# Kernel optimization log

Hardware: AMD Instinct MI355X
Metric: run time of the kernel (lower is better)

## Reference

```python
import jax, jax.numpy as jnp
import numpy as np

B, H, S, D = 1, 16, 2048, 128
SINK = 4            # SINK_LENGTH in source
QMAX = 7.0          # 4-bit symmetric: 2**(4-1)-1
K_OUT = 8           # outlier tokens kept per (b,h,d) channel slice (outlier_dim=-2)
V_OUT = 4           # outlier channels kept per (b,h,s) token slice (outlier_dim=-1)


def setup_inputs() -> dict:
    key = jax.random.key(0)
    kq, kk, kv = jax.random.split(key, 3)
    return {
        "q_tensor": jax.random.normal(kq, (B, H, S, D), jnp.float32),
        "k_tensor": jax.random.normal(kk, (B, H, S, D), jnp.float32),
        "v_tensor": jax.random.normal(kv, (B, H, S, D), jnp.float32),
    }


def _causal_attention(q, k, v):
    # standard SDPA, prefill chunk (cache empty), no RoPE (rotary_emb_module is None)
    scores = jnp.einsum("bhqd,bhkd->bhqk", q, k) * (D ** -0.5)
    causal = jnp.tril(jnp.ones((S, S), bool))
    scores = jnp.where(causal, scores, -1e30)
    probs = jax.nn.softmax(scores, axis=-1)
    return jnp.einsum("bhqk,bhkd->bhqd", probs, v)


def _isolate_k(x, n):
    # outlier_dim=-2: per (b,h,d) channel slice, pull top-n |.| tokens out as sparse
    xt = jnp.transpose(x, (0, 1, 3, 2))                     # [B,H,D,S]
    _, idx = jax.lax.top_k(jnp.abs(xt), n)                  # [B,H,D,n] token indices
    vals = jnp.take_along_axis(xt, idx, axis=-1)            # [B,H,D,n]
    bb = jnp.arange(B)[:, None, None, None]
    hh = jnp.arange(H)[None, :, None, None]
    dd = jnp.arange(D)[None, None, :, None]
    dense = jnp.transpose(xt.at[bb, hh, dd, idx].set(0.0), (0, 1, 3, 2))
    flat_idx = ((bb * H + hh) * S + idx) * D + dd           # flat index into [B,H,S,D]
    return dense, vals.reshape(-1), flat_idx.reshape(-1)


def _isolate_v(x, n):
    # outlier_dim=-1: per (b,h,s) token slice, pull top-n |.| channels out as sparse
    _, idx = jax.lax.top_k(jnp.abs(x), n)                   # [B,H,S,n] channel indices
    vals = jnp.take_along_axis(x, idx, axis=-1)
    bb = jnp.arange(B)[:, None, None, None]
    hh = jnp.arange(H)[None, :, None, None]
    ss = jnp.arange(S)[None, None, :, None]
    dense = x.at[bb, hh, ss, idx].set(0.0)
    flat_idx = ((bb * H + hh) * S + ss) * D + idx
    return dense, vals.reshape(-1), flat_idx.reshape(-1)


def _quantize_dense(x, absmax):
    scale = jnp.maximum(absmax, 1e-8) / QMAX
    q = jnp.clip(jnp.round(x / scale), -QMAX, QMAX)
    return q, scale


def reference(q_tensor, k_tensor, v_tensor):
    attn_output = _causal_attention(q_tensor, k_tensor, v_tensor)

    # chunk 0 prefill: zero sink tokens before outlier isolation
    k_iso = k_tensor.at[:, :, :SINK, :].set(0.0)
    v_iso = v_tensor.at[:, :, :SINK, :].set(0.0)

    k_dense, k_sp_val, k_sp_idx = _isolate_k(k_iso, K_OUT)
    v_dense, v_sp_val, v_sp_idx = _isolate_v(v_iso, V_OUT)

    # append full-precision sink tokens as sparse entries (flat indices)
    flat_ids = jnp.arange(B * H * S * D, dtype=jnp.int32).reshape(B, H, S, D)
    sink_idx = flat_ids[:, :, :SINK, :].reshape(-1)
    v_sp_val = jnp.concatenate([v_sp_val, v_tensor[:, :, :SINK, :].reshape(-1)])
    v_sp_idx = jnp.concatenate([v_sp_idx.astype(jnp.int32), sink_idx])
    k_sp_val = jnp.concatenate([k_sp_val, k_tensor[:, :, :SINK, :].reshape(-1)])
    k_sp_idx = jnp.concatenate([k_sp_idx.astype(jnp.int32), sink_idx])

    # key stats: per-channel absmax over tokens; value stats: per-token absmax over channels
    k_absmax = jnp.max(jnp.abs(k_dense), axis=2, keepdims=True)   # [B,H,1,D]
    v_absmax = jnp.max(jnp.abs(v_dense), axis=3, keepdims=True)   # [B,H,S,1]

    k_quant, k_scale = _quantize_dense(k_dense, k_absmax)
    v_quant, v_scale = _quantize_dense(v_dense, v_absmax)

    return (attn_output,
            k_quant, k_scale, k_sp_val, k_sp_idx,
            v_quant, v_scale, v_sp_val, v_sp_idx)
```

## Files before the change

kernel.cpp:

```cpp
#include <hip/hip_runtime.h>

#define HH 16
#define SS 2048
#define DD 128

#define O0 0u
#define O1 4194304u
#define O2 8388608u
#define O3 8390656u
#define O4 8415232u
#define O5 8439808u
#define O6 12634112u
#define O7 12666880u
#define O8 12806144u

using bf16x8 = __attribute__((ext_vector_type(8))) short;
using f32x4  = __attribute__((ext_vector_type(4))) float;

static __device__ __forceinline__ unsigned short f2bf(float f) {
  union { float f; unsigned u; } x; x.f = f;
  unsigned r = x.u + 0x7fffu + ((x.u >> 16) & 1u);
  return (unsigned short)(r >> 16);
}

typedef __attribute__((address_space(1))) const unsigned int gu32_t;
typedef __attribute__((address_space(3))) unsigned int lu32_t;
static __device__ __forceinline__ void gl_lds16(const void* g, void* l) {
  __builtin_amdgcn_global_load_lds((gu32_t*)g, (lu32_t*)l, 16, 0, 0);
}

#define INS9(a_, v_, i_)                                              \
  if ((a_) > aab[8]) {                                                \
    aab[8] = (a_); av[8] = (v_); ai[8] = (i_);                        \
    _Pragma("unroll")                                                 \
    for (int jj = 8; jj > 0; --jj) {                                  \
      if (aab[jj] > aab[jj - 1]) {                                    \
        float ta = aab[jj]; aab[jj] = aab[jj - 1]; aab[jj - 1] = ta;  \
        float tv = av[jj];  av[jj]  = av[jj - 1];  av[jj - 1]  = tv;  \
        int   ti = ai[jj];  ai[jj]  = ai[jj - 1];  ai[jj - 1]  = ti;  \
      }                                                               \
    }                                                                 \
  }

#define INS5(a_, v_, i_)                                              \
  if ((a_) > ab5[4]) {                                                \
    ab5[4] = (a_); v5[4] = (v_); i5[4] = (i_);                        \
    _Pragma("unroll")                                                 \
    for (int jj = 4; jj > 0; --jj) {                                  \
      if (ab5[jj] > ab5[jj - 1]) {                                    \
        float ta = ab5[jj]; ab5[jj] = ab5[jj - 1]; ab5[jj - 1] = ta;  \
        float tv = v5[jj];  v5[jj]  = v5[jj - 1];  v5[jj - 1]  = tv;  \
        int   ti = i5[jj];  i5[jj]  = i5[jj - 1];  i5[jj - 1]  = ti;  \
      }                                                               \
    }                                                                 \
  }

__global__ __launch_bounds__(256) void prep_kv(const float* __restrict__ K,
                                               const float* __restrict__ V,
                                               uint4* __restrict__ WK,
                                               uint4* __restrict__ WV,
                                               float* __restrict__ wval,
                                               int* __restrict__ widx,
                                               float* __restrict__ out) {
  if (blockIdx.y == 0) {
    if (blockIdx.x >= 256) return;
    const int h  = blockIdx.x >> 4;
    const int sb = blockIdx.x & 15;
    const float* Kh = K + (size_t)h * (SS * DD);
    const int tid = threadIdx.x;

    for (int slot = tid; slot < 2048; slot += 256) {
      const int tl = slot >> 10, sl = slot & 1023;
      const int chunk = sl >> 6, l = sl & 63;
      const int ct = chunk >> 2, t = chunk & 3;
      const int row = (sb * 2 + tl) * 64 + ct * 16 + (l & 15);
      const float* src = Kh + (size_t)row * DD + t * 32 + (l >> 4) * 8;
      const float4 a = *(const float4*)src;
      const float4 b = *(const float4*)(src + 4);
      uint4 r;
      r.x = (unsigned)f2bf(a.x) | ((unsigned)f2bf(a.y) << 16);
      r.y = (unsigned)f2bf(a.z) | ((unsigned)f2bf(a.w) << 16);
      r.z = (unsigned)f2bf(b.x) | ((unsigned)f2bf(b.y) << 16);
      r.w = (unsigned)f2bf(b.z) | ((unsigned)f2bf(b.w) << 16);
      WK[(size_t)(h * 32 + sb * 2 + tl) * 1024 + sl] = r;
    }

    const int d   = tid & 127;
    const int sub = tid >> 7;
    const int s0  = sb * 128 + sub * 64;
    float aab[9], av[9]; int ai[9];
    #pragma unroll
    for (int j = 0; j < 9; ++j) { aab[j] = -1.f; av[j] = 0.f; ai[j] = 0; }
    for (int ib = 0; ib < 64; ib += 8) {
      float vv[8];
      #pragma unroll
      for (int u = 0; u < 8; ++u)
        vv[u] = Kh[((size_t)(s0 + ib + u) << 7) + d];
      #pragma unroll
      for (int u = 0; u < 8; ++u) {
        const int s = s0 + ib + u;
        const float v = (s < 4) ? 0.f : vv[u];
        const float a = fabsf(v);
        INS9(a, v, s)
      }
    }
    __shared__ float lv[128][9];
    __shared__ int   li[128][9];
    if (sub == 1) {
      #pragma unroll
      for (int j = 0; j < 9; ++j) { lv[d][j] = av[j]; li[d][j] = ai[j]; }
    }
    __syncthreads();
    if (sub == 0) {
      #pragma unroll
      for (int j = 0; j < 9; ++j) {
        const float v = lv[d][j];
        const int  s2 = li[d][j];
        const float a = fabsf(v);
        INS9(a, v, s2)
      }
      const int base = (sb * 2048 + h * 128 + d) * 9;
      #pragma unroll
      for (int j = 0; j < 9; ++j) { wval[base + j] = av[j]; widx[base + j] = ai[j]; }
    }
  } else {
    __shared__ float T[64][133];
    __shared__ float pv[64][4][5];
    __shared__ int   pi[64][4][5];
    __shared__ float ssc[64];
    __shared__ int   sid4[64][4];
    const int ht = blockIdx.x;
    const int h = ht >> 5;
    const int s_base = (ht & 31) * 64;
    const float* Vh = V + (size_t)h * (SS * DD) + (size_t)s_base * DD;

    for (int i = threadIdx.x; i < 2048; i += 256) {
      const int flat = i << 2;
      const int row = flat >> 7, col = flat & 127;
      const float4 a = *(const float4*)(Vh + (size_t)row * DD + col);
      T[row][col]     = a.x;
      T[row][col + 1] = a.y;
      T[row][col + 2] = a.z;
      T[row][col + 3] = a.w;
    }
    __syncthreads();

    uint4* dst = WV + (size_t)ht * 1024;
    for (int slot = threadIdx.x; slot < 1024; slot += 256) {
      const int chunk = slot >> 6, l = slot & 63;
      const int c = chunk >> 1, tk = chunk & 1;
      const int n  = c * 16 + (l & 15);
      const int k0 = tk * 32 + (l >> 4) * 8;
      unsigned short u[8];
      #pragma unroll
      for (int j = 0; j < 8; ++j) u[j] = f2bf(T[k0 + j][n]);
      uint4 r;
      r.x = (unsigned)u[0] | ((unsigned)u[1] << 16);
      r.y = (unsigned)u[2] | ((unsigned)u[3] << 16);
      r.z = (unsigned)u[4] | ((unsigned)u[5] << 16);
      r.w = (unsigned)u[6] | ((unsigned)u[7] << 16);
      dst[slot] = r;
    }

    {
      const int tok  = threadIdx.x >> 2;
      const int part = threadIdx.x & 3;
      const int sg   = s_base + tok;
      float ab5[5], v5[5]; int i5[5];
      #pragma unroll
      for (int j = 0; j < 5; ++j) { ab5[j] = -1.f; v5[j] = 0.f; i5[j] = 0; }
      for (int c = 0; c < 32; ++c) {
        const int ch = part * 32 + c;
        const float w = (sg < 4) ? 0.f : T[tok][ch];
        const float a = fabsf(w);
        INS5(a, w, ch)
      }
      #pragma unroll
      for (int j = 0; j < 5; ++j) { pv[tok][part][j] = v5[j]; pi[tok][part][j] = i5[j]; }
    }
    __syncthreads();

    if (threadIdx.x < 64) {
      const int tok = threadIdx.x;
      const int sg  = s_base + tok;
      float ab5[5], v5[5]; int i5[5];
      #pragma unroll
      for (int j = 0; j < 5; ++j) { ab5[j] = -1.f; v5[j] = 0.f; i5[j] = 0; }
      for (int part = 0; part < 4; ++part)
        #pragma unroll
        for (int j = 0; j < 5; ++j) {
          const float w = pv[tok][part][j];
          const int  ch = pi[tok][part][j];
          const float a = fabsf(w);
          INS5(a, w, ch)
        }
      const float scale = fmaxf(ab5[4], 1e-8f) / 7.0f;
      const int gw = h * SS + sg;
      out[O6 + gw] = scale;
      ssc[tok] = scale;
      #pragma unroll
      for (int j = 0; j < 4; ++j) {
        out[O7 + gw * 4 + j] = v5[j];
        out[O8 + gw * 4 + j] = (float)(gw * DD + i5[j]);
        sid4[tok][j] = i5[j];
      }
    }
    __syncthreads();

    for (int e = threadIdx.x; e < 8192; e += 256) {
      const int tok = e >> 7, ch = e & 127;
      const int sg  = s_base + tok;
      const float w = (sg < 4) ? 0.f : T[tok][ch];
      const bool z = (ch == sid4[tok][0]) | (ch == sid4[tok][1]) |
                     (ch == sid4[tok][2]) | (ch == sid4[tok][3]);
      const float q = z ? 0.f : fminf(7.f, fmaxf(-7.f, rintf(w / ssc[tok])));
      out[O5 + (size_t)(h * SS + sg) * DD + ch] = q;
    }
  }
}

__global__ __launch_bounds__(256) void attn_ws(const float* __restrict__ Q,
                                               const uint4* __restrict__ WK,
                                               const uint4* __restrict__ WV,
                                               float* __restrict__ O) {
  const int bid = blockIdx.x;
  const int x  = bid & 7;
  const int kk = bid >> 3;
  const int p  = kk >> 5;
  const int r  = kk & 31;
  const int h  = x * 2 + (r & 1);
  const int jj = r >> 1;
  const int qb = p ? (31 - jj) : jj;
  const int q0 = qb << 6;
  const int tid = threadIdx.x;
  const int w   = tid >> 6;
  const int l   = tid & 63;
  const int l15 = l & 15;
  const int lg  = l >> 4;

  __shared__ uint4 Kt[2][1024];
  __shared__ uint4 Vt[2][1024];
  __shared__ unsigned short Pl[4][16][72];

  bf16x8 qf[4];
  {
    const float* qp = Q + (size_t)h * (SS * DD) + (size_t)(q0 + w * 16 + l15) * DD + lg * 8;
    #pragma unroll
    for (int t = 0; t < 4; ++t) {
      const float4 a = *(const float4*)(qp + t * 32);
      const float4 b = *(const float4*)(qp + t * 32 + 4);
      bf16x8 f;
      f[0] = (short)f2bf(a.x); f[1] = (short)f2bf(a.y);
      f[2] = (short)f2bf(a.z); f[3] = (short)f2bf(a.w);
      f[4] = (short)f2bf(b.x); f[5] = (short)f2bf(b.y);
      f[6] = (short)f2bf(b.z); f[7] = (short)f2bf(b.w);
      qf[t] = f;
    }
  }

  f32x4 acc[8];
  #pragma unroll
  for (int c = 0; c < 8; ++c) acc[c] = (f32x4){0.f, 0.f, 0.f, 0.f};
  float mrow = -1e30f, lrow = 0.f;

  const float sc2 = 0.08838834764831845f * 1.4426950408889634f;

  {
    const size_t tbase = (size_t)(h * 32) * 1024;
    #pragma unroll
    for (int i = 0; i < 4; ++i) {
      const int ch = (w << 2) + i;
      gl_lds16(WK + tbase + ch * 64 + l, &Kt[0][ch * 64]);
      gl_lds16(WV + tbase + ch * 64 + l, &Vt[0][ch * 64]);
    }
  }
  __syncthreads();

  for (int kt = 0; kt <= qb; ++kt) {
    const int cur = kt & 1;

    if (kt < qb) {
      const size_t tbase = (size_t)(h * 32 + kt + 1) * 1024;
      #pragma unroll
      for (int i = 0; i < 4; ++i) {
        const int ch = (w << 2) + i;
        gl_lds16(WK + tbase + ch * 64 + l, &Kt[cur ^ 1][ch * 64]);
        gl_lds16(WV + tbase + ch * 64 + l, &Vt[cur ^ 1][ch * 64]);
      }
    }

    const bool diag = (kt == qb);
    const int ctmax = diag ? (w + 1) : 4;

    float p[4][4];
    float mt = -1e30f;
    __builtin_amdgcn_s_setprio(1);
    #pragma unroll
    for (int ct = 0; ct < 4; ++ct) {
      if (ct < ctmax) {
        f32x4 a = (f32x4){0.f, 0.f, 0.f, 0.f};
        #pragma unroll
        for (int t = 0; t < 4; ++t) {
          bf16x8 kb = ((const bf16x8*)Kt[cur])[(ct * 4 + t) * 64 + l];
          a = __builtin_amdgcn_mfma_f32_16x16x32_bf16(kb, qf[t], a, 0, 0, 0);
        }
        #pragma unroll
        for (int r2 = 0; r2 < 4; ++r2) {
          float s = a[r2] * sc2;
          if (diag) {
            const int koff = ct * 16 + lg * 4 + r2;
            s = (koff > w * 16 + l15) ? -1e30f : s;
          }
          p[ct][r2] = s;
          mt = fmaxf(mt, s);
        }
      }
    }
    __builtin_amdgcn_s_setprio(0);

    mt = fmaxf(mt, __shfl_xor(mt, 16));
    mt = fmaxf(mt, __shfl_xor(mt, 32));
    const float mn = fmaxf(mrow, mt);

    float rs = 0.f;
    #pragma unroll
    for (int ct = 0; ct < 4; ++ct) {
      if (ct < ctmax) {
        #pragma unroll
        for (int r2 = 0; r2 < 4; ++r2) {
          const float e = exp2f(p[ct][r2] - mn);
          p[ct][r2] = e;
          rs += e;
        }
      } else {
        #pragma unroll
        for (int r2 = 0; r2 < 4; ++r2) p[ct][r2] = 0.f;
      }
    }
    rs += __shfl_xor(rs, 16);
    rs += __shfl_xor(rs, 32);

    if (__any(mt > mrow)) {
      const float al = exp2f(mrow - mn);
      float alr[4];
      #pragma unroll
      for (int r2 = 0; r2 < 4; ++r2) alr[r2] = __shfl(al, lg * 4 + r2);
      #pragma unroll
      for (int c = 0; c < 8; ++c)
        #pragma unroll
        for (int r2 = 0; r2 < 4; ++r2) acc[c][r2] *= alr[r2];
      lrow = lrow * al + rs;
      mrow = mn;
    } else {
      lrow += rs;
    }

    #pragma unroll
    for (int ct = 0; ct < 4; ++ct) {
      uint2 pk;
      pk.x = (unsigned)f2bf(p[ct][0]) | ((unsigned)f2bf(p[ct][1]) << 16);
      pk.y = (unsigned)f2bf(p[ct][2]) | ((unsigned)f2bf(p[ct][3]) << 16);
      *(uint2*)&Pl[w][l15][ct * 16 + lg * 4] = pk;
    }

    __builtin_amdgcn_s_setprio(1);
    #pragma unroll
    for (int tk = 0; tk < 2; ++tk) {
      bf16x8 pa = *(const bf16x8*)&Pl[w][l15][tk * 32 + lg * 8];
      #pragma unroll
      for (int c = 0; c < 8; ++c) {
        bf16x8 vb = ((const bf16x8*)Vt[cur])[(c * 2 + tk) * 64 + l];
        acc[c] = __builtin_amdgcn_mfma_f32_16x16x32_bf16(pa, vb, acc[c], 0, 0, 0);
      }
    }
    __builtin_amdgcn_s_setprio(0);

    __syncthreads();
  }

  const float inv = 1.0f / lrow;
  float invr[4];
  #pragma unroll
  for (int r2 = 0; r2 < 4; ++r2) invr[r2] = __shfl(inv, lg * 4 + r2);
  #pragma unroll
  for (int r2 = 0; r2 < 4; ++r2) {
    const int row = q0 + w * 16 + lg * 4 + r2;
    float* op = O + O0 + (size_t)(h * SS + row) * DD;
    #pragma unroll
    for (int c = 0; c < 8; ++c)
      op[c * 16 + l15] = acc[c][r2] * invr[r2];
  }
}

__global__ __launch_bounds__(256) void attn_fb(const float* __restrict__ Q,
                                               const float* __restrict__ K,
                                               const float* __restrict__ V,
                                               float* __restrict__ O) {
  const int h   = blockIdx.x >> 5;
  const int q0  = (blockIdx.x & 31) << 6;
  const int tid = threadIdx.x;
  const int w   = tid >> 6;
  const int l   = tid & 63;
  const int l15 = l & 15;
  const int lg  = l >> 4;

  __shared__ unsigned short Kl[64][136];
  __shared__ unsigned short Vt[128][72];
  __shared__ unsigned short Pl[4][16][72];

  const size_t hbase = (size_t)h * (SS * DD);
  const float* Qh = Q + hbase;
  const float* Kh = K + hbase;
  const float* Vh = V + hbase;

  bf16x8 qf[4];
  {
    const float* qp = Qh + (size_t)(q0 + w * 16 + l15) * DD + lg * 8;
    #pragma unroll
    for (int t = 0; t < 4; ++t) {
      bf16x8 f;
      #pragma unroll
      for (int j = 0; j < 8; ++j) f[j] = (short)f2bf(qp[t * 32 + j]);
      qf[t] = f;
    }
  }

  f32x4 acc[8];
  #pragma unroll
  for (int c = 0; c < 8; ++c) acc[c] = (f32x4){0.f, 0.f, 0.f, 0.f};
  float mrow[4], lrow[4];
  #pragma unroll
  for (int r = 0; r < 4; ++r) { mrow[r] = -1e30f; lrow[r] = 0.f; }

  const float sc2 = 0.08838834764831845f * 1.4426950408889634f;

  const int ntile = (q0 >> 6) + 1;
  for (int kt = 0; kt < ntile; ++kt) {
    const int kv0 = kt << 6;
    __syncthreads();
    for (int idx = tid; idx < 64 * 128; idx += 256) {
      const int kv = idx >> 7, d = idx & 127;
      const size_t g = (size_t)(kv0 + kv) * DD + d;
      Kl[kv][d] = f2bf(Kh[g]);
      Vt[d][kv] = f2bf(Vh[g]);
    }
    __syncthreads();

    f32x4 sacc[4];
    #pragma unroll
    for (int ct = 0; ct < 4; ++ct) {
      f32x4 a = (f32x4){0.f, 0.f, 0.f, 0.f};
      #pragma unroll
      for (int t = 0; t < 4; ++t) {
        bf16x8 kb = *(const bf16x8*)&Kl[ct * 16 + l15][t * 32 + lg * 8];
        a = __builtin_amdgcn_mfma_f32_16x16x32_bf16(qf[t], kb, a, 0, 0, 0);
      }
      sacc[ct] = a;
    }

    float sv[4][4];
    #pragma unroll
    for (int ct = 0; ct < 4; ++ct) {
      const int col = kv0 + ct * 16 + l15;
      #pragma unroll
      for (int r = 0; r < 4; ++r) {
        const int row = q0 + w * 16 + lg * 4 + r;
        sv[ct][r] = (col > row) ? -1e30f : sacc[ct][r] * sc2;
      }
    }

    #pragma unroll
    for (int r = 0; r < 4; ++r) {
      float mt = fmaxf(fmaxf(sv[0][r], sv[1][r]), fmaxf(sv[2][r], sv[3][r]));
      #pragma unroll
      for (int m = 1; m < 16; m <<= 1) mt = fmaxf(mt, __shfl_xor(mt, m));
      const float mn = fmaxf(mrow[r], mt);
      const float al = exp2f(mrow[r] - mn);
      mrow[r] = mn;
      float rs = 0.f;
      #pragma unroll
      for (int ct = 0; ct < 4; ++ct) {
        const float p = exp2f(sv[ct][r] - mn);
        sv[ct][r] = p;
        rs += p;
      }
      #pragma unroll
      for (int m = 1; m < 16; m <<= 1) rs += __shfl_xor(rs, m);
      lrow[r] = lrow[r] * al + rs;
      #pragma unroll
      for (int c = 0; c < 8; ++c) acc[c][r] *= al;
    }

    #pragma unroll
    for (int ct = 0; ct < 4; ++ct)
      #pragma unroll
      for (int r = 0; r < 4; ++r)
        Pl[w][lg * 4 + r][ct * 16 + l15] = f2bf(sv[ct][r]);

    #pragma unroll
    for (int tk = 0; tk < 2; ++tk) {
      bf16x8 pa = *(const bf16x8*)&Pl[w][l15][tk * 32 + lg * 8];
      #pragma unroll
      for (int c = 0; c < 8; ++c) {
        bf16x8 vb = *(const bf16x8*)&Vt[c * 16 + l15][tk * 32 + lg * 8];
        acc[c] = __builtin_amdgcn_mfma_f32_16x16x32_bf16(pa, vb, acc[c], 0, 0, 0);
      }
    }
  }

  #pragma unroll
  for (int r = 0; r < 4; ++r) {
    const float inv = 1.0f / lrow[r];
    const int row = q0 + w * 16 + lg * 4 + r;
    float* op = O + O0 + (size_t)(h * SS + row) * DD;
    #pragma unroll
    for (int c = 0; c < 8; ++c)
      op[c * 16 + l15] = acc[c][r] * inv;
  }
}

__global__ __launch_bounds__(256) void v_kernel(const float* __restrict__ V,
                                                float* __restrict__ out) {
  const int gw = (blockIdx.x << 2) + (threadIdx.x >> 6);
  const int l  = threadIdx.x & 63;
  const int s  = gw & (SS - 1);
  const float2 v2 = ((const float2*)(V + (size_t)gw * DD))[l];
  const bool sink = (s < 4);
  const float w0 = sink ? 0.f : v2.x;
  const float w1 = sink ? 0.f : v2.y;
  float a0 = fabsf(w0), a1 = fabsf(w1);
  const int d0 = 2 * l, d1 = 2 * l + 1;

  float oval[4]; int oidx[4]; float scale = 0.f;
  #pragma unroll
  for (int rnd = 0; rnd < 5; ++rnd) {
    float ba; int bd; float bv;
    if (a1 > a0) { ba = a1; bd = d1; bv = w1; }
    else         { ba = a0; bd = d0; bv = w0; }
    #pragma unroll
    for (int m = 1; m < 64; m <<= 1) {
      const float oa = __shfl_xor(ba, m);
      const int   od = __shfl_xor(bd, m);
      const float ov = __shfl_xor(bv, m);
      if (oa > ba || (oa == ba && od < bd)) { ba = oa; bd = od; bv = ov; }
    }
    if (rnd < 4) {
      oval[rnd] = bv; oidx[rnd] = bd;
      if (bd == d0) a0 = -1.f;
      if (bd == d1) a1 = -1.f;
    } else {
      scale = fmaxf(ba, 1e-8f) / 7.0f;
    }
  }

  const bool z0 = (oidx[0] == d0) | (oidx[1] == d0) | (oidx[2] == d0) | (oidx[3] == d0);
  const bool z1 = (oidx[0] == d1) | (oidx[1] == d1) | (oidx[2] == d1) | (oidx[3] == d1);
  const float q0 = z0 ? 0.f : fminf(7.f, fmaxf(-7.f, rintf(w0 / scale)));
  const float q1 = z1 ? 0.f : fminf(7.f, fmaxf(-7.f, rintf(w1 / scale)));
  float2 pack; pack.x = q0; pack.y = q1;
  *(float2*)(out + O5 + (size_t)gw * DD + d0) = pack;

  if (l == 0) {
    out[O6 + gw] = scale;
    #pragma unroll
    for (int j = 0; j < 4; ++j) {
      out[O7 + gw * 4 + j] = oval[j];
      out[O8 + gw * 4 + j] = (float)(gw * DD + oidx[j]);
    }
  }
}

__global__ __launch_bounds__(64) void k_merge(const float* __restrict__ wval,
                                              const int* __restrict__ widx,
                                              const float* __restrict__ K,
                                              const float* __restrict__ V,
                                              float* __restrict__ out) {
  const int ch = blockIdx.x * 64 + threadIdx.x;
  const int h = ch >> 7, d = ch & 127;

  float aab[9], av[9]; int ai[9];
  #pragma unroll
  for (int j = 0; j < 9; ++j) { aab[j] = -1.f; av[j] = 0.f; ai[j] = 0; }

  float va[9], vb[9]; int ia[9], ib[9];
  {
    const int b0 = ch * 9;
    #pragma unroll
    for (int j = 0; j < 9; ++j) { va[j] = wval[b0 + j]; ia[j] = widx[b0 + j]; }
  }

  for (int sb = 0; sb < 16; ++sb) {
    if (sb < 15) {
      const int nb = ((sb + 1) * 2048 + ch) * 9;
      #pragma unroll
      for (int j = 0; j < 9; ++j) { vb[j] = wval[nb + j]; ib[j] = widx[nb + j]; }
    }
    #pragma unroll
    for (int j = 0; j < 9; ++j) {
      const float v = va[j];
      const int  si = ia[j];
      const float a = fabsf(v);
      INS9(a, v, si)
    }
    #pragma unroll
    for (int j = 0; j < 9; ++j) { va[j] = vb[j]; ia[j] = ib[j]; }
  }

  const float scale = fmaxf(aab[8], 1e-8f) / 7.0f;
  out[O2 + ch] = scale;
  #pragma unroll
  for (int j = 0; j < 8; ++j) {
    out[O3 + ch * 8u + j] = av[j];
    out[O4 + ch * 8u + j] = (float)((h * SS + ai[j]) * DD + d);
  }

  #pragma unroll
  for (int u = 0; u < 4; ++u) {
    const int i  = ch * 4 + u;
    const int hh = i >> 9;
    const int r  = i & 511;
    const int flat = hh * (SS * DD) + r;
    const float fidx = (float)flat;
    out[O3 + 16384u + i]  = K[flat];
    out[O4 + 16384u + i]  = fidx;
    out[O7 + 131072u + i] = V[flat];
    out[O8 + 131072u + i] = fidx;
  }
}

__global__ __launch_bounds__(256) void k_top(const float* __restrict__ K,
                                             float* __restrict__ out) {
  const int h  = blockIdx.x;
  const int t  = threadIdx.x;
  const int st = t >> 7;
  const float* Kh = K + (size_t)h * (SS * DD);

  __shared__ float lv[256][9];
  __shared__ int   li[256][9];

  float aab[9], av[9]; int ai[9];
  #pragma unroll
  for (int j = 0; j < 9; ++j) { aab[j] = -1.f; av[j] = 0.f; ai[j] = 0; }

  const int d = t & 127;
  const int s0 = st << 10;
  for (int i = 0; i < 1024; ++i) {
    const int s = s0 + i;
    float v = Kh[((size_t)s << 7) + d];
    if (s < 4) v = 0.f;
    const float a = fabsf(v);
    INS9(a, v, s)
  }

  #pragma unroll
  for (int j = 0; j < 9; ++j) { lv[t][j] = av[j]; li[t][j] = ai[j]; }
  __syncthreads();

  if (t < 128) {
    #pragma unroll
    for (int j = 0; j < 9; ++j) {
      const float v = lv[t + 128][j];
      const int  s2 = li[t + 128][j];
      const float a = fabsf(v);
      INS9(a, v, s2)
    }
    const float scale = fmaxf(aab[8], 1e-8f) / 7.0f;
    const unsigned ch = (unsigned)(h * 128 + t);
    out[O2 + ch] = scale;
    #pragma unroll
    for (int j = 0; j < 8; ++j) {
      out[O3 + ch * 8u + j] = av[j];
      out[O4 + ch * 8u + j] = (float)((h * SS + ai[j]) * DD + t);
    }
  }
}

__global__ __launch_bounds__(256) void sink_kernel(const float* __restrict__ K,
                                                   const float* __restrict__ V,
                                                   float* __restrict__ out) {
  const int i = blockIdx.x * 256 + threadIdx.x;
  const int h = i >> 9;
  const int r = i & 511;
  const int flat = h * (SS * DD) + r;
  const float fidx = (float)flat;
  out[O3 + 16384u + i]  = K[flat];
  out[O4 + 16384u + i]  = fidx;
  out[O7 + 131072u + i] = V[flat];
  out[O8 + 131072u + i] = fidx;
}

__global__ __launch_bounds__(256) void k_quant(const float* __restrict__ K,
                                               const float* __restrict__ outr,
                                               float* __restrict__ out) {
  __shared__ float ssc[128];
  __shared__ int   sid[128][8];
  const int e0 = blockIdx.x * 1024;
  const int h  = e0 >> 18;
  if (threadIdx.x < 128) {
    const unsigned ch = (unsigned)(h * 128 + threadIdx.x);
    ssc[threadIdx.x] = outr[O2 + ch];
    #pragma unroll
    for (int j = 0; j < 8; ++j)
      sid[threadIdx.x][j] = ((int)outr[O4 + ch * 8u + j] >> 7) & (SS - 1);
  }
  __syncthreads();

  const int e  = e0 + threadIdx.x * 4;
  const int dd = e & 127;
  const int s  = (e >> 7) & (SS - 1);
  const float4 kv = *(const float4*)(K + e);
  const float vv[4] = {kv.x, kv.y, kv.z, kv.w};
  float4 res;
  float rr[4];
  #pragma unroll
  for (int jj = 0; jj < 4; ++jj) {
    const int d = dd + jj;
    bool zero = (s < 4);
    #pragma unroll
    for (int j = 0; j < 8; ++j) zero |= (sid[d][j] == s);
    rr[jj] = zero ? 0.f : fminf(7.f, fmaxf(-7.f, rintf(vv[jj] / ssc[d])));
  }
  res.x = rr[0]; res.y = rr[1]; res.z = rr[2]; res.w = rr[3];
  *(float4*)(out + O1 + e) = res;
}

extern "C" void kernel_launch(void* const* d_in, const int* in_sizes, int n_in,
                              void* d_out, int out_size, void* d_ws, size_t ws_size,
                              hipStream_t stream) {
  const float* q = (const float*)d_in[0];
  const float* k = (const float*)d_in[1];
  const float* v = (const float*)d_in[2];
  float* out = (float*)d_out;

  const size_t nBF   = 524288;
  const size_t nPart = (size_t)2048 * 16 * 9;
  const size_t needFull = nBF * 2 * sizeof(uint4) + nPart * 8;

  uint4* wsk = (uint4*)d_ws;
  uint4* wsv = wsk + nBF;
  float* wval = (float*)(wsv + nBF);
  int*   widx = (int*)(wval + nPart);

  if (ws_size >= needFull) {
    prep_kv<<<dim3(512, 2), dim3(256), 0, stream>>>(k, v, wsk, wsv, wval, widx, out);
    attn_ws<<<dim3(512), dim3(256), 0, stream>>>(q, wsk, wsv, out);
    k_merge<<<dim3(32), dim3(64), 0, stream>>>(wval, widx, k, v, out);
  } else {
    attn_fb<<<dim3(512), dim3(256), 0, stream>>>(q, k, v, out);
    v_kernel<<<dim3(HH * SS / 4), dim3(256), 0, stream>>>(v, out);
    k_top<<<dim3(HH), dim3(256), 0, stream>>>(k, out);
    sink_kernel<<<dim3(32), dim3(256), 0, stream>>>(k, v, out);
  }
  k_quant<<<dim3(4096), dim3(256), 0, stream>>>(k, out, out);
}
```

Measured before the change: 202.0 us.

## Split fused K/V prep kernel and move V top-k quantization to warp-per-token kernel

The combined prep_kv kernel is split into prep_k (K bf16 packing plus partial top-k) and prep_v (V bf16 transpose-pack only). V outlier extraction and quantization move to the existing warp-per-token v_kernel, which now runs after attention. The aim is to take the serial per-token insertion sorts and the extra block syncs out of the prep stage so attention's inputs are ready sooner. The cost is one more kernel launch and V being read from global memory a second time.

```diff
diff --git a/kernel.cpp b/kernel.cpp
--- a/kernel.cpp
+++ b/kernel.cpp
@@ -42,179 +42,153 @@
     }                                                                 \
   }
 
-#define INS5(a_, v_, i_)                                              \
-  if ((a_) > ab5[4]) {                                                \
-    ab5[4] = (a_); v5[4] = (v_); i5[4] = (i_);                        \
-    _Pragma("unroll")                                                 \
-    for (int jj = 4; jj > 0; --jj) {                                  \
-      if (ab5[jj] > ab5[jj - 1]) {                                    \
-        float ta = ab5[jj]; ab5[jj] = ab5[jj - 1]; ab5[jj - 1] = ta;  \
-        float tv = v5[jj];  v5[jj]  = v5[jj - 1];  v5[jj - 1]  = tv;  \
-        int   ti = i5[jj];  i5[jj]  = i5[jj - 1];  i5[jj - 1]  = ti;  \
-      }                                                               \
-    }                                                                 \
-  }
-
-__global__ __launch_bounds__(256) void prep_kv(const float* __restrict__ K,
-                                               const float* __restrict__ V,
-                                               uint4* __restrict__ WK,
-                                               uint4* __restrict__ WV,
-                                               float* __restrict__ wval,
-                                               int* __restrict__ widx,
-                                               float* __restrict__ out) {
-  if (blockIdx.y == 0) {
-    if (blockIdx.x >= 256) return;
-    const int h  = blockIdx.x >> 4;
-    const int sb = blockIdx.x & 15;
-    const float* Kh = K + (size_t)h * (SS * DD);
-    const int tid = threadIdx.x;
-
-    for (int slot = tid; slot < 2048; slot += 256) {
-      const int tl = slot >> 10, sl = slot & 1023;
-      const int chunk = sl >> 6, l = sl & 63;
-      const int ct = chunk >> 2, t = chunk & 3;
-      const int row = (sb * 2 + tl) * 64 + ct * 16 + (l & 15);
-      const float* src = Kh + (size_t)row * DD + t * 32 + (l >> 4) * 8;
-      const float4 a = *(const float4*)src;
-      const float4 b = *(const float4*)(src + 4);
-      uint4 r;
-      r.x = (unsigned)f2bf(a.x) | ((unsigned)f2bf(a.y) << 16);
-      r.y = (unsigned)f2bf(a.z) | ((unsigned)f2bf(a.w) << 16);
-      r.z = (unsigned)f2bf(b.x) | ((unsigned)f2bf(b.y) << 16);
-      r.w = (unsigned)f2bf(b.z) | ((unsigned)f2bf(b.w) << 16);
-      WK[(size_t)(h * 32 + sb * 2 + tl) * 1024 + sl] = r;
-    }
-
-    const int d   = tid & 127;
-    const int sub = tid >> 7;
-    const int s0  = sb * 128 + sub * 64;
-    float aab[9], av[9]; int ai[9];
-    #pragma unroll
-    for (int j = 0; j < 9; ++j) { aab[j] = -1.f; av[j] = 0.f; ai[j] = 0; }
-    for (int ib = 0; ib < 64; ib += 8) {
-      float vv[8];
-      #pragma unroll
-      for (int u = 0; u < 8; ++u)
-        vv[u] = Kh[((size_t)(s0 + ib + u) << 7) + d];
-      #pragma unroll
-      for (int u = 0; u < 8; ++u) {
-        const int s = s0 + ib + u;
-        const float v = (s < 4) ? 0.f : vv[u];
-        const float a = fabsf(v);
-        INS9(a, v, s)
-      }
-    }
-    __shared__ float lv[128][9];
-    __shared__ int   li[128][9];
-    if (sub == 1) {
-      #pragma unroll
-      for (int j = 0; j < 9; ++j) { lv[d][j] = av[j]; li[d][j] = ai[j]; }
-    }
-    __syncthreads();
-    if (sub == 0) {
-      #pragma unroll
-      for (int j = 0; j < 9; ++j) {
-        const float v = lv[d][j];
-        const int  s2 = li[d][j];
-        const float a = fabsf(v);
-        INS9(a, v, s2)
-      }
-      const int base = (sb * 2048 + h * 128 + d) * 9;
-      #pragma unroll
-      for (int j = 0; j < 9; ++j) { wval[base + j] = av[j]; widx[base + j] = ai[j]; }
-    }
-  } else {
-    __shared__ float T[64][133];
-    __shared__ float pv[64][4][5];
-    __shared__ int   pi[64][4][5];
-    __shared__ float ssc[64];
-    __shared__ int   sid4[64][4];
-    const int ht = blockIdx.x;
-    const int h = ht >> 5;
-    const int s_base = (ht & 31) * 64;
-    const float* Vh = V + (size_t)h * (SS * DD) + (size_t)s_base * DD;
-
-    for (int i = threadIdx.x; i < 2048; i += 256) {
-      const int flat = i << 2;
-      const int row = flat >> 7, col = flat & 127;
-      const float4 a = *(const float4*)(Vh + (size_t)row * DD + col);
-      T[row][col]     = a.x;
-      T[row][col + 1] = a.y;
-      T[row][col + 2] = a.z;
-      T[row][col + 3] = a.w;
-    }
-    __syncthreads();
-
-    uint4* dst = WV + (size_t)ht * 1024;
-    for (int slot = threadIdx.x; slot < 1024; slot += 256) {
-      const int chunk = slot >> 6, l = slot & 63;
-      const int c = chunk >> 1, tk = chunk & 1;
-      const int n  = c * 16 + (l & 15);
-      const int k0 = tk * 32 + (l >> 4) * 8;
-      unsigned short u[8];
-      #pragma unroll
-      for (int j = 0; j < 8; ++j) u[j] = f2bf(T[k0 + j][n]);
-      uint4 r;
-      r.x = (unsigned)u[0] | ((unsigned)u[1] << 16);
-      r.y = (unsigned)u[2] | ((unsigned)u[3] << 16);
-      r.z = (unsigned)u[4] | ((unsigned)u[5] << 16);
-      r.w = (unsigned)u[6] | ((unsigned)u[7] << 16);
-      dst[slot] = r;
-    }
-
-    {
-      const int tok  = threadIdx.x >> 2;
-      const int part = threadIdx.x & 3;
-      const int sg   = s_base + tok;
-      float ab5[5], v5[5]; int i5[5];
-      #pragma unroll
-      for (int j = 0; j < 5; ++j) { ab5[j] = -1.f; v5[j] = 0.f; i5[j] = 0; }
-      for (int c = 0; c < 32; ++c) {
-        const int ch = part * 32 + c;
-        const float w = (sg < 4) ? 0.f : T[tok][ch];
-        const float a = fabsf(w);
-        INS5(a, w, ch)
-      }
-      #pragma unroll
-      for (int j = 0; j < 5; ++j) { pv[tok][part][j] = v5[j]; pi[tok][part][j] = i5[j]; }
-    }
-    __syncthreads();
-
-    if (threadIdx.x < 64) {
-      const int tok = threadIdx.x;
-      const int sg  = s_base + tok;
-      float ab5[5], v5[5]; int i5[5];
-      #pragma unroll
-      for (int j = 0; j < 5; ++j) { ab5[j] = -1.f; v5[j] = 0.f; i5[j] = 0; }
-      for (int part = 0; part < 4; ++part)
-        #pragma unroll
-        for (int j = 0; j < 5; ++j) {
-          const float w = pv[tok][part][j];
-          const int  ch = pi[tok][part][j];
-          const float a = fabsf(w);
-          INS5(a, w, ch)
-        }
-      const float scale = fmaxf(ab5[4], 1e-8f) / 7.0f;
-      const int gw = h * SS + sg;
-      out[O6 + gw] = scale;
-      ssc[tok] = scale;
-      #pragma unroll
-      for (int j = 0; j < 4; ++j) {
-        out[O7 + gw * 4 + j] = v5[j];
-        out[O8 + gw * 4 + j] = (float)(gw * DD + i5[j]);
-        sid4[tok][j] = i5[j];
-      }
-    }
-    __syncthreads();
-
-    for (int e = threadIdx.x; e < 8192; e += 256) {
-      const int tok = e >> 7, ch = e & 127;
-      const int sg  = s_base + tok;
-      const float w = (sg < 4) ? 0.f : T[tok][ch];
-      const bool z = (ch == sid4[tok][0]) | (ch == sid4[tok][1]) |
-                     (ch == sid4[tok][2]) | (ch == sid4[tok][3]);
-      const float q = z ? 0.f : fminf(7.f, fmaxf(-7.f, rintf(w / ssc[tok])));
-      out[O5 + (size_t)(h * SS + sg) * DD + ch] = q;
+__global__ __launch_bounds__(256) void prep_k(const float* __restrict__ K,
+                                              uint4* __restrict__ WK,
+                                              float* __restrict__ wval,
+                                              int* __restrict__ widx) {
+  const int h  = blockIdx.x >> 4;
+  const int sb = blockIdx.x & 15;
+  const float* Kh = K + (size_t)h * (SS * DD);
+  const int tid = threadIdx.x;
+
+  for (int slot = tid; slot < 2048; slot += 256) {
+    const int tl = slot >> 10, sl = slot & 1023;
+    const int chunk = sl >> 6, l = sl & 63;
+    const int ct = chunk >> 2, t = chunk & 3;
+    const int row = (sb * 2 + tl) * 64 + ct * 16 + (l & 15);
+    const float* src = Kh + (size_t)row * DD + t * 32 + (l >> 4) * 8;
+    const float4 a = *(const float4*)src;
+    const float4 b = *(const float4*)(src + 4);
+    uint4 r;
+    r.x = (unsigned)f2bf(a.x) | ((unsigned)f2bf(a.y) << 16);
+    r.y = (unsigned)f2bf(a.z) | ((unsigned)f2bf(a.w) << 16);
+    r.z = (unsigned)f2bf(b.x) | ((unsigned)f2bf(b.y) << 16);
+    r.w = (unsigned)f2bf(b.z) | ((unsigned)f2bf(b.w) << 16);
+    WK[(size_t)(h * 32 + sb * 2 + tl) * 1024 + sl] = r;
+  }
+
+  const int d   = tid & 127;
+  const int sub = tid >> 7;
+  const int s0  = sb * 128 + sub * 64;
+  float aab[9], av[9]; int ai[9];
+  #pragma unroll
+  for (int j = 0; j < 9; ++j) { aab[j] = -1.f; av[j] = 0.f; ai[j] = 0; }
+  for (int ib = 0; ib < 64; ib += 8) {
+    float vv[8];
+    #pragma unroll
+    for (int u = 0; u < 8; ++u)
+      vv[u] = Kh[((size_t)(s0 + ib + u) << 7) + d];
+    #pragma unroll
+    for (int u = 0; u < 8; ++u) {
+      const int s = s0 + ib + u;
+      const float v = (s < 4) ? 0.f : vv[u];
+      const float a = fabsf(v);
+      INS9(a, v, s)
+    }
+  }
+  __shared__ float lv[128][9];
+  __shared__ int   li[128][9];
+  if (sub == 1) {
+    #pragma unroll
+    for (int j = 0; j < 9; ++j) { lv[d][j] = av[j]; li[d][j] = ai[j]; }
+  }
+  __syncthreads();
+  if (sub == 0) {
+    #pragma unroll
+    for (int j = 0; j < 9; ++j) {
+      const float v = lv[d][j];
+      const int  s2 = li[d][j];
+      const float a = fabsf(v);
+      INS9(a, v, s2)
+    }
+    const int base = (sb * 2048 + h * 128 + d) * 9;
+    #pragma unroll
+    for (int j = 0; j < 9; ++j) { wval[base + j] = av[j]; widx[base + j] = ai[j]; }
+  }
+}
+
+__global__ __launch_bounds__(256) void prep_v(const float* __restrict__ V,
+                                              uint4* __restrict__ WV) {
+  __shared__ float T[64][133];
+  const int ht = blockIdx.x;
+  const float* Vh = V + (size_t)(ht >> 5) * (SS * DD) + (size_t)(ht & 31) * 64 * DD;
+
+  for (int i = threadIdx.x; i < 2048; i += 256) {
+    const int flat = i << 2;
+    const int row = flat >> 7, col = flat & 127;
+    const float4 a = *(const float4*)(Vh + (size_t)row * DD + col);
+    T[row][col]     = a.x;
+    T[row][col + 1] = a.y;
+    T[row][col + 2] = a.z;
+    T[row][col + 3] = a.w;
+  }
+  __syncthreads();
+
+  uint4* dst = WV + (size_t)ht * 1024;
+  for (int slot = threadIdx.x; slot < 1024; slot += 256) {
+    const int chunk = slot >> 6, l = slot & 63;
+    const int c = chunk >> 1, tk = chunk & 1;
+    const int n  = c * 16 + (l & 15);
+    const int k0 = tk * 32 + (l >> 4) * 8;
+    unsigned short u[8];
+    #pragma unroll
+    for (int j = 0; j < 8; ++j) u[j] = f2bf(T[k0 + j][n]);
+    uint4 r;
+    r.x = (unsigned)u[0] | ((unsigned)u[1] << 16);
+    r.y = (unsigned)u[2] | ((unsigned)u[3] << 16);
+    r.z = (unsigned)u[4] | ((unsigned)u[5] << 16);
+    r.w = (unsigned)u[6] | ((unsigned)u[7] << 16);
+    dst[slot] = r;
+  }
+}
+
+__global__ __launch_bounds__(256) void v_kernel(const float* __restrict__ V,
+                                                float* __restrict__ out) {
+  const int gw = (blockIdx.x << 2) + (threadIdx.x >> 6);
+  const int l  = threadIdx.x & 63;
+  const int s  = gw & (SS - 1);
+  const float2 v2 = ((const float2*)(V + (size_t)gw * DD))[l];
+  const bool sink = (s < 4);
+  const float w0 = sink ? 0.f : v2.x;
+  const float w1 = sink ? 0.f : v2.y;
+  float a0 = fabsf(w0), a1 = fabsf(w1);
+  const int d0 = 2 * l, d1 = 2 * l + 1;
+
+  float oval[4]; int oidx[4]; float scale = 0.f;
+  #pragma unroll
+  for (int rnd = 0; rnd < 5; ++rnd) {
+    float ba; int bd; float bv;
+    if (a1 > a0) { ba = a1; bd = d1; bv = w1; }
+    else         { ba = a0; bd = d0; bv = w0; }
+    #pragma unroll
+    for (int m = 1; m < 64; m <<= 1) {
+      const float oa = __shfl_xor(ba, m);
+      const int   od = __shfl_xor(bd, m);
+      const float ov = __shfl_xor(bv, m);
+      if (oa > ba || (oa == ba && od < bd)) { ba = oa; bd = od; bv = ov; }
+    }
+    if (rnd < 4) {
+      oval[rnd] = bv; oidx[rnd] = bd;
+      if (bd == d0) a0 = -1.f;
+      if (bd == d1) a1 = -1.f;
+    } else {
+      scale = fmaxf(ba, 1e-8f) / 7.0f;
+    }
+  }
+
+  const bool z0 = (oidx[0] == d0) | (oidx[1] == d0) | (oidx[2] == d0) | (oidx[3] == d0);
+  const bool z1 = (oidx[0] == d1) | (oidx[1] == d1) | (oidx[2] == d1) | (oidx[3] == d1);
+  const float q0 = z0 ? 0.f : fminf(7.f, fmaxf(-7.f, rintf(w0 / scale)));
+  const float q1 = z1 ? 0.f : fminf(7.f, fmaxf(-7.f, rintf(w1 / scale)));
+  float2 pack; pack.x = q0; pack.y = q1;
+  *(float2*)(out + O5 + (size_t)gw * DD + d0) = pack;
+
+  if (l == 0) {
+    out[O6 + gw] = scale;
+    #pragma unroll
+    for (int j = 0; j < 4; ++j) {
+      out[O7 + gw * 4 + j] = oval[j];
+      out[O8 + gw * 4 + j] = (float)(gw * DD + oidx[j]);
     }
   }
 }
@@ -519,57 +493,6 @@
   }
 }
 
-__global__ __launch_bounds__(256) void v_kernel(const float* __restrict__ V,
-                                                float* __restrict__ out) {
-  const int gw = (blockIdx.x << 2) + (threadIdx.x >> 6);
-  const int l  = threadIdx.x & 63;
-  const int s  = gw & (SS - 1);
-  const float2 v2 = ((const float2*)(V + (size_t)gw * DD))[l];
-  const bool sink = (s < 4);
-  const float w0 = sink ? 0.f : v2.x;
-  const float w1 = sink ? 0.f : v2.y;
-  float a0 = fabsf(w0), a1 = fabsf(w1);
-  const int d0 = 2 * l, d1 = 2 * l + 1;
-
-  float oval[4]; int oidx[4]; float scale = 0.f;
-  #pragma unroll
-  for (int rnd = 0; rnd < 5; ++rnd) {
-    float ba; int bd; float bv;
-    if (a1 > a0) { ba = a1; bd = d1; bv = w1; }
-    else         { ba = a0; bd = d0; bv = w0; }
-    #pragma unroll
-    for (int m = 1; m < 64; m <<= 1) {
-      const float oa = __shfl_xor(ba, m);
-      const int   od = __shfl_xor(bd, m);
-      const float ov = __shfl_xor(bv, m);
-      if (oa > ba || (oa == ba && od < bd)) { ba = oa; bd = od; bv = ov; }
-    }
-    if (rnd < 4) {
-      oval[rnd] = bv; oidx[rnd] = bd;
-      if (bd == d0) a0 = -1.f;
-      if (bd == d1) a1 = -1.f;
-    } else {
-      scale = fmaxf(ba, 1e-8f) / 7.0f;
-    }
-  }
-
-  const bool z0 = (oidx[0] == d0) | (oidx[1] == d0) | (oidx[2] == d0) | (oidx[3] == d0);
-  const bool z1 = (oidx[0] == d1) | (oidx[1] == d1) | (oidx[2] == d1) | (oidx[3] == d1);
-  const float q0 = z0 ? 0.f : fminf(7.f, fmaxf(-7.f, rintf(w0 / scale)));
-  const float q1 = z1 ? 0.f : fminf(7.f, fmaxf(-7.f, rintf(w1 / scale)));
-  float2 pack; pack.x = q0; pack.y = q1;
-  *(float2*)(out + O5 + (size_t)gw * DD + d0) = pack;
-
-  if (l == 0) {
-    out[O6 + gw] = scale;
-    #pragma unroll
-    for (int j = 0; j < 4; ++j) {
-      out[O7 + gw * 4 + j] = oval[j];
-      out[O8 + gw * 4 + j] = (float)(gw * DD + oidx[j]);
-    }
-  }
-}
-
 __global__ __launch_bounds__(64) void k_merge(const float* __restrict__ wval,
                                               const int* __restrict__ widx,
                                               const float* __restrict__ K,
@@ -742,8 +665,10 @@
   int*   widx = (int*)(wval + nPart);
 
   if (ws_size >= needFull) {
-    prep_kv<<<dim3(512, 2), dim3(256), 0, stream>>>(k, v, wsk, wsv, wval, widx, out);
+    prep_k<<<dim3(256), dim3(256), 0, stream>>>(k, wsk, wval, widx);
+    prep_v<<<dim3(512), dim3(256), 0, stream>>>(v, wsv);
     attn_ws<<<dim3(512), dim3(256), 0, stream>>>(q, wsk, wsv, out);
+    v_kernel<<<dim3(HH * SS / 4), dim3(256), 0, stream>>>(v, out);
     k_merge<<<dim3(32), dim3(64), 0, stream>>>(wval, widx, k, v, out);
   } else {
     attn_fb<<<dim3(512), dim3(256), 0, stream>>>(q, k, v, out);
```

Measured after the change: 235.9 us. 16.7% more time.
